# Optimization experiments

Hardware: AMD Instinct MI355X
Metric: run time of the kernel (lower is better)

Reference implementation:

```python
import jax, jax.numpy as jnp
import numpy as np

EMBED_DIM = 1024
N_HEADS = 16
HEAD_DIM = EMBED_DIM // N_HEADS
BATCH = 2
SEQ = 2048


def setup_inputs() -> dict:
    key = jax.random.key(0)
    ks = jax.random.split(key, 12)
    s = 1.0 / np.sqrt(EMBED_DIM)
    return {
        "x": jax.random.normal(ks[0], (BATCH, SEQ, EMBED_DIM), jnp.float32),
        "q_w": jax.random.normal(ks[1], (EMBED_DIM, EMBED_DIM), jnp.float32) * s,
        "q_b": jax.random.normal(ks[2], (EMBED_DIM,), jnp.float32) * s,
        "k_w": jax.random.normal(ks[3], (EMBED_DIM, EMBED_DIM), jnp.float32) * s,
        "k_b": jax.random.normal(ks[4], (EMBED_DIM,), jnp.float32) * s,
        "v_w": jax.random.normal(ks[5], (EMBED_DIM, EMBED_DIM), jnp.float32) * s,
        "v_b": jax.random.normal(ks[6], (EMBED_DIM,), jnp.float32) * s,
        "phase": jax.random.normal(ks[7], (N_HEADS, HEAD_DIM), jnp.float32),
        "entanglement": jax.random.normal(ks[8], (N_HEADS, HEAD_DIM, HEAD_DIM), jnp.float32) * 0.1,
        "out_w": jax.random.normal(ks[9], (EMBED_DIM, EMBED_DIM), jnp.float32) * s,
        "out_b": jax.random.normal(ks[10], (EMBED_DIM,), jnp.float32) * s,
    }


def reference(x, q_w, q_b, k_w, k_b, v_w, v_b, phase, entanglement, out_w, out_b):
    b, s, _ = x.shape
    # projections -> [b, h, s, d]
    def split_heads(y):
        return y.reshape(b, s, N_HEADS, HEAD_DIM).transpose(0, 2, 1, 3)
    Q = split_heads(x @ q_w + q_b)
    K = split_heads(x @ k_w + k_b)
    V = split_heads(x @ v_w + v_b)
    # real part of phase-rotated Q/K: Q * cos(phase) (imag discarded by .real)
    cosp = jnp.cos(phase)[None, :, None, :]  # [1, h, 1, d]
    Qc = Q * cosp
    Kc = K * cosp
    scores = jnp.einsum('bhqd,bhkd->bhqk', Qc, Kc) / np.sqrt(HEAD_DIM)
    # bilinear entanglement term: Q . E . K^T per head
    scores = scores + jnp.einsum('bhqd,hde,bhke->bhqk', Q, entanglement, K)
    attn = jax.nn.softmax(scores, axis=-1)
    attended = jnp.einsum('bhqk,bhkd->bhqd', attn, V)
    attended = attended.transpose(0, 2, 1, 3).reshape(b, s, EMBED_DIM)
    return attended @ out_w + out_b
```

## Files before the change

### kernel.cpp

```cpp
#include <hip/hip_runtime.h>
#include <hip/hip_bf16.h>

typedef __bf16 bf16;
typedef __bf16 bf16x8 __attribute__((ext_vector_type(8)));
typedef __bf16 bf16x4 __attribute__((ext_vector_type(4)));
typedef float f32x4 __attribute__((ext_vector_type(4)));
typedef float f32x16 __attribute__((ext_vector_type(16)));
typedef unsigned int u32x2 __attribute__((ext_vector_type(2)));

#define EMBED 1024
#define NH 16
#define HD 64
#define BATCH 2
#define SEQ 2048
#define MTOK 4096
#define LOG2E 1.4426950408889634f

static __device__ __forceinline__ float fast_exp2(float x) {
#if __has_builtin(__builtin_amdgcn_exp2f)
  return __builtin_amdgcn_exp2f(x);
#else
  float r;
  asm("v_exp_f32 %0, %1" : "=v"(r) : "v"(x));
  return r;
#endif
}

static __device__ __forceinline__ f32x4 mfma16(bf16x8 a, bf16x8 b, f32x4 c) {
  return __builtin_amdgcn_mfma_f32_16x16x32_bf16(a, b, c, 0, 0, 0);
}
static __device__ __forceinline__ f32x16 mfma32(bf16x8 a, bf16x8 b, f32x16 c) {
  return __builtin_amdgcn_mfma_f32_32x32x16_bf16(a, b, c, 0, 0, 0);
}

static __device__ __forceinline__ void gld_lds16(const bf16* g, bf16* l) {
  __builtin_amdgcn_global_load_lds(
      (const __attribute__((address_space(1))) void*)g,
      (__attribute__((address_space(3))) void*)l, 16, 0, 0);
}

__global__ __launch_bounds__(256) void prep_kernel(
    const float* __restrict__ x, const float* __restrict__ qw,
    const float* __restrict__ qb, const float* __restrict__ kw,
    const float* __restrict__ vw, const float* __restrict__ ow,
    const float* __restrict__ ent, const float* __restrict__ phase,
    bf16* __restrict__ xb, bf16* __restrict__ wtall, bf16* __restrict__ wot,
    float* __restrict__ beff) {
  __shared__ float t0[64][65];
  __shared__ float t1[64][65];
  const int bb = blockIdx.x;
  const int tid = threadIdx.x;

  if (bb < 2048) {
    const int n4 = MTOK * EMBED / 4;
    int i = bb * 256 + tid;
    for (; i < n4; i += 2048 * 256) {
      f32x4 v = ((const f32x4*)x)[i];
      bf16x4 o;
      o[0] = (bf16)v[0]; o[1] = (bf16)v[1]; o[2] = (bf16)v[2]; o[3] = (bf16)v[3];
      ((bf16x4*)xb)[i] = o;
    }
    return;
  }
  if (bb < 2816) {
    const int idx = (bb - 2048) & 255;
    const float* W = (bb < 2304) ? kw : (bb < 2560) ? vw : ow;
    bf16* Wt = (bb < 2304) ? (wtall + 1024 * 1024)
             : (bb < 2560) ? (wtall + 2 * 1024 * 1024) : wot;
    const int bc = (idx & 15) * 64;
    const int br = (idx >> 4) * 64;
#pragma unroll
    for (int j = 0; j < 16; j++) {
      int id2 = j * 256 + tid;
      int r = id2 >> 6, c = id2 & 63;
      t0[r][c] = W[(size_t)(br + r) * EMBED + bc + c];
    }
    __syncthreads();
#pragma unroll
    for (int j = 0; j < 16; j++) {
      int id2 = j * 256 + tid;
      int r = id2 >> 6, c = id2 & 63;
      Wt[(size_t)(bc + r) * EMBED + br + c] = (bf16)t0[c][r];
    }
    return;
  }
  if (bb < 3072) {
    const int idx = bb - 2816;
    const int h = idx >> 4;
    const int ibase = (idx & 15) * 64;
#pragma unroll
    for (int j = 0; j < 16; j++) {
      int id2 = j * 256 + tid;
      int i = id2 >> 6, d = id2 & 63;
      t0[i][d] = qw[(size_t)(ibase + i) * EMBED + h * HD + d];
    }
#pragma unroll
    for (int j = 0; j < 16; j++) {
      int id2 = j * 256 + tid;
      int d = id2 >> 6, e = id2 & 63;
      float v = ent[((size_t)h * HD + d) * HD + e];
      if (d == e) { float cp = cosf(phase[h * HD + d]); v += cp * cp * 0.125f; }
      t1[d][e] = v * LOG2E;
    }
    __syncthreads();
    const int i = tid & 63;
    const int e0 = (tid >> 6) * 16;
    float s[16];
#pragma unroll
    for (int ee = 0; ee < 16; ee++) s[ee] = 0.f;
    for (int d = 0; d < 64; d++) {
      float qv = t0[i][d];
#pragma unroll
      for (int ee = 0; ee < 16; ee++) s[ee] += qv * t1[d][e0 + ee];
    }
#pragma unroll
    for (int ee = 0; ee < 16; ee++)
      wtall[(size_t)(h * HD + e0 + ee) * EMBED + ibase + i] = (bf16)s[ee];
    return;
  }
  const int h = bb - 3072;
  if (tid < 64) {
    const int e = tid;
    float s = 0.f;
    for (int d = 0; d < 64; d++) {
      float v = ent[((size_t)h * HD + d) * HD + e];
      if (d == e) { float cp = cosf(phase[h * HD + d]); v += cp * cp * 0.125f; }
      s += qb[h * HD + d] * v;
    }
    beff[h * HD + e] = s * LOG2E;
  }
}

__global__ __launch_bounds__(256, 4) void gemm_qkv_kernel(
    const bf16* __restrict__ A, const bf16* __restrict__ Bt,
    const float* __restrict__ bias_q, const float* __restrict__ bias_k,
    const float* __restrict__ bias_v,
    bf16* __restrict__ Qp, bf16* __restrict__ Kp, bf16* __restrict__ Vt) {
  const int tid = threadIdx.x;
  const int lane = tid & 63, w = tid >> 6;
  const int g = lane >> 4, r15 = lane & 15;
  const int wr = w >> 1, wc = w & 1;

  const int flat = blockIdx.x;
  const int bm = (flat & 31) * 128;
  const int bn = (flat >> 5) * 128;
  const int seg = bn >> 10;

  __shared__ bf16 sA[128 * 32];
  __shared__ bf16 sB[128 * 32];

  const int srow = tid >> 2;
  const int scol = (tid & 3) << 3;
  const bf16* aptr = A + (size_t)(bm + srow) * EMBED + scol;
  const bf16* bptr = Bt + (size_t)(bn + srow) * EMBED + scol;
  bf16* la = sA + tid * 8;
  bf16* lb = sB + tid * 8;

  if (seg == 2) {
    f32x4 acc[4][4];
#pragma unroll
    for (int m = 0; m < 4; m++)
#pragma unroll
      for (int n = 0; n < 4; n++) acc[m][n] = (f32x4){0.f, 0.f, 0.f, 0.f};

    for (int k0 = 0; k0 < EMBED; k0 += 32) {
      __syncthreads();
      gld_lds16(aptr + k0, la);
      gld_lds16(aptr + k0 + 64 * EMBED, la + 64 * 32);
      gld_lds16(bptr + k0, lb);
      gld_lds16(bptr + k0 + 64 * EMBED, lb + 64 * 32);
      __syncthreads();
      bf16x8 af[4], bfv[4];
#pragma unroll
      for (int m = 0; m < 4; m++)
        af[m] = *(const bf16x8*)&sA[(wr * 64 + m * 16 + r15) * 32 + g * 8];
#pragma unroll
      for (int n = 0; n < 4; n++)
        bfv[n] = *(const bf16x8*)&sB[(wc * 64 + n * 16 + r15) * 32 + g * 8];
#pragma unroll
      for (int m = 0; m < 4; m++)
#pragma unroll
        for (int n = 0; n < 4; n++) acc[m][n] = mfma16(af[m], bfv[n], acc[m][n]);
    }

    const int clb = (bn & 1023) + wc * 64;
    const int orow0 = bm + wr * 64;
#pragma unroll
    for (int n = 0; n < 4; n++) {
      const int cl = clb + n * 16 + r15;
      const float bias = bias_v[cl];
      const int hh = cl >> 6, d = cl & 63;
#pragma unroll
      for (int m = 0; m < 4; m++) {
        const int row0 = orow0 + m * 16 + g * 4;
        const int b = row0 >> 11, s = row0 & 2047;
        bf16x4 pk;
#pragma unroll
        for (int r = 0; r < 4; r++) pk[r] = (bf16)(acc[m][n][r] + bias);
        *(bf16x4*)(Vt + ((size_t)((b * NH + hh) * HD + d)) * SEQ + s) = pk;
      }
    }
  } else {
    f32x4 acc[4][4];
#pragma unroll
    for (int m = 0; m < 4; m++)
#pragma unroll
      for (int n = 0; n < 4; n++) acc[m][n] = (f32x4){0.f, 0.f, 0.f, 0.f};

    for (int k0 = 0; k0 < EMBED; k0 += 32) {
      __syncthreads();
      gld_lds16(aptr + k0, la);
      gld_lds16(aptr + k0 + 64 * EMBED, la + 64 * 32);
      gld_lds16(bptr + k0, lb);
      gld_lds16(bptr + k0 + 64 * EMBED, lb + 64 * 32);
      __syncthreads();
      bf16x8 af[4], bfv[4];
#pragma unroll
      for (int m = 0; m < 4; m++)
        af[m] = *(const bf16x8*)&sA[(wr * 64 + m * 16 + r15) * 32 + g * 8];
#pragma unroll
      for (int n = 0; n < 4; n++)
        bfv[n] = *(const bf16x8*)&sB[(wc * 64 + n * 16 + r15) * 32 + g * 8];
#pragma unroll
      for (int m = 0; m < 4; m++)
#pragma unroll
        for (int n = 0; n < 4; n++) acc[m][n] = mfma16(bfv[n], af[m], acc[m][n]);
    }

    const float* bias = seg ? bias_k : bias_q;
    bf16* dst = seg ? Kp : Qp;
    const int clb = (bn & 1023) + wc * 64;
#pragma unroll
    for (int n = 0; n < 4; n++) {
      const int cl4 = clb + n * 16 + g * 4;
      const f32x4 b4 = *(const f32x4*)&bias[cl4];
#pragma unroll
      for (int m = 0; m < 4; m++) {
        const int tr = bm + wr * 64 + m * 16 + r15;
        bf16x4 pk;
#pragma unroll
        for (int r = 0; r < 4; r++) pk[r] = (bf16)(acc[m][n][r] + b4[r]);
        *(bf16x4*)(dst + (size_t)tr * EMBED + cl4) = pk;
      }
    }
  }
}

__global__ __launch_bounds__(256, 4) void gemm_out_kernel(
    const bf16* __restrict__ A, const bf16* __restrict__ Bt,
    const float* __restrict__ bias_o, float* __restrict__ FO) {
  const int tid = threadIdx.x;
  const int lane = tid & 63, w = tid >> 6;
  const int g = lane >> 4, r15 = lane & 15;

  const int flat = blockIdx.x;
  const int bm = (flat & 63) * 64;
  const int bn = (flat >> 6) * 128;

  __shared__ bf16 sA[64 * 32];
  __shared__ bf16 sB[128 * 32];

  f32x4 acc[4][2];
#pragma unroll
  for (int m = 0; m < 4; m++)
#pragma unroll
    for (int n = 0; n < 2; n++) acc[m][n] = (f32x4){0.f, 0.f, 0.f, 0.f};

  const int srow = tid >> 2;
  const int scol = (tid & 3) << 3;
  const bf16* aptr = A + (size_t)(bm + srow) * EMBED + scol;
  const bf16* bptr = Bt + (size_t)(bn + srow) * EMBED + scol;
  bf16* la = sA + tid * 8;
  bf16* lb = sB + tid * 8;

  for (int k0 = 0; k0 < EMBED; k0 += 32) {
    __syncthreads();
    gld_lds16(aptr + k0, la);
    gld_lds16(bptr + k0, lb);
    gld_lds16(bptr + k0 + 64 * EMBED, lb + 64 * 32);
    __syncthreads();
    bf16x8 af[4], bfv[2];
#pragma unroll
    for (int m = 0; m < 4; m++)
      af[m] = *(const bf16x8*)&sA[(m * 16 + r15) * 32 + g * 8];
#pragma unroll
    for (int n = 0; n < 2; n++)
      bfv[n] = *(const bf16x8*)&sB[(w * 32 + n * 16 + r15) * 32 + g * 8];
#pragma unroll
    for (int m = 0; m < 4; m++)
#pragma unroll
      for (int n = 0; n < 2; n++) acc[m][n] = mfma16(bfv[n], af[m], acc[m][n]);
  }

#pragma unroll
  for (int n = 0; n < 2; n++) {
    const int cl4 = bn + w * 32 + n * 16 + g * 4;
    const f32x4 b4 = *(const f32x4*)&bias_o[cl4];
#pragma unroll
    for (int m = 0; m < 4; m++) {
      const int tr = bm + m * 16 + r15;
      *(f32x4*)(FO + (size_t)tr * EMBED + cl4) = acc[m][n] + b4;
    }
  }
}

__global__ __launch_bounds__(512, 4) void flash_attn_kernel(
    const bf16* __restrict__ Qp, const bf16* __restrict__ Kp,
    const bf16* __restrict__ Vt, bf16* __restrict__ Op) {
  const int tid = threadIdx.x, lane = tid & 63, w = tid >> 6;
  const int q31 = lane & 31, hi = lane >> 5;
  const int half = w >> 2, wq = w & 3;
  const int flat = blockIdx.x;
  const int c = (flat & 7) * 64 + (flat >> 3);
  const int bh = c >> 4, qt = c & 15;
  const int b = bh >> 4, h = bh & 15;

  __shared__ char smem[65536];
  bf16* sKb = (bf16*)smem;
  bf16* sVb = (bf16*)(smem + 32768);

  const int g256 = tid & 255;
  const int strow = g256 >> 3;
  const int stcb = (g256 & 7) << 4;

  const char* kgbase = (const char*)(Kp + ((size_t)b * SEQ) * EMBED + h * HD);
  const char* vgbase = (const char*)(Vt + (size_t)bh * HD * SEQ);

  auto stage = [&](int buf, int kv0) {
    bf16* kd = sKb + (size_t)(half * 2 + buf) * 4096 + g256 * 8;
    bf16* vd = sVb + (size_t)(half * 2 + buf) * 4096 + g256 * 8;
#pragma unroll
    for (int i = 0; i < 2; i++) {
      const int row = i * 32 + strow;
      const int sb = stcb ^ ((row & 7) << 4);
      gld_lds16((const bf16*)(kgbase + (size_t)(kv0 + row) * (EMBED * 2) + sb),
                kd + i * 2048);
      gld_lds16((const bf16*)(vgbase + (size_t)row * (SEQ * 2) + (size_t)kv0 * 2 + sb),
                vd + i * 2048);
    }
  };

  const int kvbase = half * 1024;
  stage(0, kvbase);

  const int qbase = qt * 128 + wq * 32;
  const int qrow = qbase + q31;
  const bf16* qptr = Qp + ((size_t)(b * SEQ + qrow)) * EMBED + h * HD;
  bf16x8 aq[4];
#pragma unroll
  for (int ds = 0; ds < 4; ds++)
    aq[ds] = *(const bf16x8*)(qptr + ds * 16 + hi * 8);

  const int sz = (q31 & 7) << 4;
  int cofs[4];
#pragma unroll
  for (int i = 0; i < 4; i++) cofs[i] = ((i * 32 + hi * 16) ^ sz);

  f32x16 o0, o1;
#pragma unroll
  for (int i = 0; i < 16; i++) { o0[i] = 0.f; o1[i] = 0.f; }
  float mrow = -3.0e38f, lrow = 0.f;

  union B4 { bf16x4 v; unsigned int u[2]; };

  for (int it = 0; it < 16; ++it) {
    const int cur = it & 1;
    if (it + 1 < 16) {
      stage(cur ^ 1, kvbase + (it + 1) * 64);
      asm volatile("s_waitcnt vmcnt(4)" ::: "memory");
    } else {
      asm volatile("s_waitcnt vmcnt(0)" ::: "memory");
    }
    __builtin_amdgcn_s_barrier();

    const char* kc = (const char*)(sKb + (size_t)(half * 2 + cur) * 4096) + q31 * 128;
    const char* vc = (const char*)(sVb + (size_t)(half * 2 + cur) * 4096) + q31 * 128;

    f32x16 s0, s1;
#pragma unroll
    for (int i = 0; i < 16; i++) { s0[i] = 0.f; s1[i] = 0.f; }
    __builtin_amdgcn_s_setprio(1);
#pragma unroll
    for (int ds = 0; ds < 4; ds++) {
      bf16x8 bk0 = *(const bf16x8*)(kc + cofs[ds]);
      bf16x8 bk1 = *(const bf16x8*)(kc + 4096 + cofs[ds]);
      s0 = mfma32(bk0, aq[ds], s0);
      s1 = mfma32(bk1, aq[ds], s1);
    }
    __builtin_amdgcn_s_setprio(0);

    float mt = s0[0];
#pragma unroll
    for (int i = 1; i < 16; i++) mt = fmaxf(mt, s0[i]);
#pragma unroll
    for (int i = 0; i < 16; i++) mt = fmaxf(mt, s1[i]);
    {
      u32x2 sm = __builtin_amdgcn_permlane32_swap(__float_as_uint(mt),
                                                  __float_as_uint(mt), false, false);
      mt = fmaxf(__uint_as_float(sm.x), __uint_as_float(sm.y));
    }
    if (__any(mt > mrow + 8.f)) {
      const float mn = fmaxf(mrow, mt);
      const float al = fast_exp2(mrow - mn);
      mrow = mn;
      lrow *= al;
      o0 *= al;
      o1 *= al;
    }

    B4 qd[8];
    float lsum = 0.f;
#pragma unroll
    for (int j = 0; j < 4; j++)
#pragma unroll
      for (int r = 0; r < 4; r++) {
        float pv = fast_exp2(s0[4 * j + r] - mrow);
        lsum += pv;
        qd[j].v[r] = (bf16)pv;
      }
#pragma unroll
    for (int j = 0; j < 4; j++)
#pragma unroll
      for (int r = 0; r < 4; r++) {
        float pv = fast_exp2(s1[4 * j + r] - mrow);
        lsum += pv;
        qd[4 + j].v[r] = (bf16)pv;
      }
    {
      u32x2 ss = __builtin_amdgcn_permlane32_swap(__float_as_uint(lsum),
                                                  __float_as_uint(lsum), false, false);
      lrow += __uint_as_float(ss.x) + __uint_as_float(ss.y);
    }

    bf16x8 pfrag[4];
#pragma unroll
    for (int kt = 0; kt < 4; kt++) {
      u32x2 p0 = __builtin_amdgcn_permlane32_swap(qd[2 * kt].u[0],
                                                  qd[2 * kt + 1].u[0], false, false);
      u32x2 p1 = __builtin_amdgcn_permlane32_swap(qd[2 * kt].u[1],
                                                  qd[2 * kt + 1].u[1], false, false);
      union { unsigned int u[4]; bf16x8 v; } f;
      f.u[0] = p0.x; f.u[1] = p1.x; f.u[2] = p0.y; f.u[3] = p1.y;
      pfrag[kt] = f.v;
    }

    __builtin_amdgcn_s_setprio(1);
#pragma unroll
    for (int kt = 0; kt < 4; kt++) {
      bf16x8 av0 = *(const bf16x8*)(vc + cofs[kt]);
      bf16x8 av1 = *(const bf16x8*)(vc + 4096 + cofs[kt]);
      o0 = mfma32(av0, pfrag[kt], o0);
      o1 = mfma32(av1, pfrag[kt], o1);
    }
    __builtin_amdgcn_s_setprio(0);
    __builtin_amdgcn_s_barrier();
  }

  float* shO = (float*)smem;
  float* shML = (float*)(smem + 33792);
  if (half == 1) {
    float* o = shO + (size_t)(wq * 64 + lane) * 33;
#pragma unroll
    for (int i = 0; i < 16; i++) { o[i] = o0[i]; o[16 + i] = o1[i]; }
    shML[(wq * 64 + lane) * 2] = mrow;
    shML[(wq * 64 + lane) * 2 + 1] = lrow;
  }
  __syncthreads();
  if (half == 0) {
    const float* o = shO + (size_t)(wq * 64 + lane) * 33;
    const float mB = shML[(wq * 64 + lane) * 2];
    const float lB = shML[(wq * 64 + lane) * 2 + 1];
    const float M = fmaxf(mrow, mB);
    const float wA = fast_exp2(mrow - M), wB = fast_exp2(mB - M);
    const float inv = 1.f / (lrow * wA + lB * wB);
    const float fA = wA * inv, fB = wB * inv;

    bf16* obase = Op + ((size_t)(b * SEQ + qrow)) * EMBED + h * HD;
#pragma unroll
    for (int j = 0; j < 4; j++) {
      bf16x4 st;
#pragma unroll
      for (int r = 0; r < 4; r++)
        st[r] = (bf16)(o0[4 * j + r] * fA + o[4 * j + r] * fB);
      *(bf16x4*)(obase + 8 * j + 4 * hi) = st;
    }
#pragma unroll
    for (int j = 0; j < 4; j++) {
      bf16x4 st;
#pragma unroll
      for (int r = 0; r < 4; r++)
        st[r] = (bf16)(o1[4 * j + r] * fA + o[16 + 4 * j + r] * fB);
      *(bf16x4*)(obase + 32 + 8 * j + 4 * hi) = st;
    }
  }
}

extern "C" void kernel_launch(void* const* d_in, const int* in_sizes, int n_in,
                              void* d_out, int out_size, void* d_ws, size_t ws_size,
                              hipStream_t stream) {
  const float* x     = (const float*)d_in[0];
  const float* q_w   = (const float*)d_in[1];
  const float* q_b   = (const float*)d_in[2];
  const float* k_w   = (const float*)d_in[3];
  const float* k_b   = (const float*)d_in[4];
  const float* v_w   = (const float*)d_in[5];
  const float* v_b   = (const float*)d_in[6];
  const float* phase = (const float*)d_in[7];
  const float* ent   = (const float*)d_in[8];
  const float* out_w = (const float*)d_in[9];
  const float* out_b = (const float*)d_in[10];
  float* out = (float*)d_out;

  char* ws = (char*)d_ws;
  bf16* xb    = (bf16*)(ws + 0);
  bf16* wtall = (bf16*)(ws + 8388608);
  bf16* wot   = (bf16*)(ws + 14680064);
  float* beff = (float*)(ws + 16777216);
  bf16* Qp    = (bf16*)(ws + 16781312);
  bf16* Kp    = (bf16*)(ws + 25169920);
  bf16* Vt    = (bf16*)(ws + 33558528);
  (void)in_sizes; (void)n_in; (void)out_size; (void)ws_size;

  prep_kernel<<<3088, 256, 0, stream>>>(x, q_w, q_b, k_w, v_w, out_w, ent, phase,
                                        xb, wtall, wot, beff);

  gemm_qkv_kernel<<<768, 256, 0, stream>>>(
      xb, wtall, beff, k_b, v_b, Qp, Kp, Vt);

  flash_attn_kernel<<<512, 512, 0, stream>>>(Qp, Kp, Vt, xb);

  gemm_out_kernel<<<512, 256, 0, stream>>>(xb, wot, out_b, out);
}
```

Before: 136.1 us.

## Software-pipeline QK^T of next tile with softmax and PV of current tile

Restructures the attention inner loop so the QK^T MFMAs for tile it+1 are issued before the softmax and PV work of tile it, using two ping-ponged score register sets and a loop unrolled by two. K and V staging are split so each buffer is refilled as soon as its last reader is done. Exponentiation, permlane packing and PV MFMAs are interleaved per k-subtile, and the row max becomes a tree reduction to shorten dependency chains. In exchange it uses more registers, which could lower occupancy. It also waits on vmcnt(0) every iteration, which may expose global-load latency the previous vmcnt(4) scheme partly hid.

Result: slower. 154.7 us (+13.6%).

```diff
diff --git a/kernel.cpp b/kernel.cpp
--- a/kernel.cpp
+++ b/kernel.cpp
@@ -326,22 +326,28 @@
   const char* kgbase = (const char*)(Kp + ((size_t)b * SEQ) * EMBED + h * HD);
   const char* vgbase = (const char*)(Vt + (size_t)bh * HD * SEQ);
 
-  auto stage = [&](int buf, int kv0) {
+  auto stageK = [&](int buf, int kv0) {
     bf16* kd = sKb + (size_t)(half * 2 + buf) * 4096 + g256 * 8;
-    bf16* vd = sVb + (size_t)(half * 2 + buf) * 4096 + g256 * 8;
 #pragma unroll
     for (int i = 0; i < 2; i++) {
       const int row = i * 32 + strow;
       const int sb = stcb ^ ((row & 7) << 4);
       gld_lds16((const bf16*)(kgbase + (size_t)(kv0 + row) * (EMBED * 2) + sb),
                 kd + i * 2048);
+    }
+  };
+  auto stageV = [&](int buf, int kv0) {
+    bf16* vd = sVb + (size_t)(half * 2 + buf) * 4096 + g256 * 8;
+#pragma unroll
+    for (int i = 0; i < 2; i++) {
+      const int row = i * 32 + strow;
+      const int sb = stcb ^ ((row & 7) << 4);
       gld_lds16((const bf16*)(vgbase + (size_t)row * (SEQ * 2) + (size_t)kv0 * 2 + sb),
                 vd + i * 2048);
     }
   };
 
   const int kvbase = half * 1024;
-  stage(0, kvbase);
 
   const int qbase = qt * 128 + wq * 32;
   const int qrow = qbase + q31;
@@ -363,37 +369,40 @@
 
   union B4 { bf16x4 v; unsigned int u[2]; };
 
-  for (int it = 0; it < 16; ++it) {
-    const int cur = it & 1;
-    if (it + 1 < 16) {
-      stage(cur ^ 1, kvbase + (it + 1) * 64);
-      asm volatile("s_waitcnt vmcnt(4)" ::: "memory");
-    } else {
-      asm volatile("s_waitcnt vmcnt(0)" ::: "memory");
-    }
-    __builtin_amdgcn_s_barrier();
-
-    const char* kc = (const char*)(sKb + (size_t)(half * 2 + cur) * 4096) + q31 * 128;
-    const char* vc = (const char*)(sVb + (size_t)(half * 2 + cur) * 4096) + q31 * 128;
-
-    f32x16 s0, s1;
-#pragma unroll
-    for (int i = 0; i < 16; i++) { s0[i] = 0.f; s1[i] = 0.f; }
+  auto qk = [&](int it, f32x16& x0, f32x16& x1) {
+    const char* kc = (const char*)(sKb + (size_t)(half * 2 + (it & 1)) * 4096)
+                     + q31 * 128;
+    f32x16 z0, z1;
+#pragma unroll
+    for (int i = 0; i < 16; i++) { z0[i] = 0.f; z1[i] = 0.f; }
     __builtin_amdgcn_s_setprio(1);
 #pragma unroll
     for (int ds = 0; ds < 4; ds++) {
       bf16x8 bk0 = *(const bf16x8*)(kc + cofs[ds]);
       bf16x8 bk1 = *(const bf16x8*)(kc + 4096 + cofs[ds]);
-      s0 = mfma32(bk0, aq[ds], s0);
-      s1 = mfma32(bk1, aq[ds], s1);
+      z0 = mfma32(bk0, aq[ds], z0);
+      z1 = mfma32(bk1, aq[ds], z1);
     }
     __builtin_amdgcn_s_setprio(0);
-
-    float mt = s0[0];
-#pragma unroll
-    for (int i = 1; i < 16; i++) mt = fmaxf(mt, s0[i]);
-#pragma unroll
-    for (int i = 0; i < 16; i++) mt = fmaxf(mt, s1[i]);
+    x0 = z0;
+    x1 = z1;
+  };
+
+  auto smpv = [&](int it, f32x16& c0, f32x16& c1) {
+    float t[11];
+#pragma unroll
+    for (int i = 0; i < 5; i++)
+      t[i] = fmaxf(fmaxf(c0[3 * i], c0[3 * i + 1]), c0[3 * i + 2]);
+    t[5] = fmaxf(fmaxf(c0[15], c1[0]), c1[1]);
+#pragma unroll
+    for (int i = 0; i < 4; i++)
+      t[6 + i] = fmaxf(fmaxf(c1[2 + 3 * i], c1[3 + 3 * i]), c1[4 + 3 * i]);
+    t[10] = fmaxf(c1[14], c1[15]);
+    const float u0 = fmaxf(fmaxf(t[0], t[1]), t[2]);
+    const float u1 = fmaxf(fmaxf(t[3], t[4]), t[5]);
+    const float u2 = fmaxf(fmaxf(t[6], t[7]), t[8]);
+    const float u3 = fmaxf(fmaxf(t[9], t[10]), u0);
+    float mt = fmaxf(fmaxf(u1, u2), u3);
     {
       u32x2 sm = __builtin_amdgcn_permlane32_swap(__float_as_uint(mt),
                                                   __float_as_uint(mt), false, false);
@@ -408,52 +417,71 @@
       o1 *= al;
     }
 
-    B4 qd[8];
+    const char* vc = (const char*)(sVb + (size_t)(half * 2 + (it & 1)) * 4096)
+                     + q31 * 128;
     float lsum = 0.f;
-#pragma unroll
-    for (int j = 0; j < 4; j++)
+    __builtin_amdgcn_s_setprio(1);
+#pragma unroll
+    for (int kt = 0; kt < 4; kt++) {
+      const f32x16& xs = (kt < 2) ? c0 : c1;
+      const int jb = (kt & 1) * 2;
+      B4 q0, q1;
 #pragma unroll
       for (int r = 0; r < 4; r++) {
-        float pv = fast_exp2(s0[4 * j + r] - mrow);
-        lsum += pv;
-        qd[j].v[r] = (bf16)pv;
+        float pa = fast_exp2(xs[4 * jb + r] - mrow);
+        float pb = fast_exp2(xs[4 * (jb + 1) + r] - mrow);
+        lsum += pa + pb;
+        q0.v[r] = (bf16)pa;
+        q1.v[r] = (bf16)pb;
       }
-#pragma unroll
-    for (int j = 0; j < 4; j++)
-#pragma unroll
-      for (int r = 0; r < 4; r++) {
-        float pv = fast_exp2(s1[4 * j + r] - mrow);
-        lsum += pv;
-        qd[4 + j].v[r] = (bf16)pv;
-      }
+      u32x2 p0 = __builtin_amdgcn_permlane32_swap(q0.u[0], q1.u[0], false, false);
+      u32x2 p1 = __builtin_amdgcn_permlane32_swap(q0.u[1], q1.u[1], false, false);
+      union { unsigned int u[4]; bf16x8 v; } f;
+      f.u[0] = p0.x; f.u[1] = p1.x; f.u[2] = p0.y; f.u[3] = p1.y;
+      bf16x8 av0 = *(const bf16x8*)(vc + cofs[kt]);
+      bf16x8 av1 = *(const bf16x8*)(vc + 4096 + cofs[kt]);
+      o0 = mfma32(av0, f.v, o0);
+      o1 = mfma32(av1, f.v, o1);
+    }
+    __builtin_amdgcn_s_setprio(0);
     {
       u32x2 ss = __builtin_amdgcn_permlane32_swap(__float_as_uint(lsum),
                                                   __float_as_uint(lsum), false, false);
       lrow += __uint_as_float(ss.x) + __uint_as_float(ss.y);
     }
-
-    bf16x8 pfrag[4];
-#pragma unroll
-    for (int kt = 0; kt < 4; kt++) {
-      u32x2 p0 = __builtin_amdgcn_permlane32_swap(qd[2 * kt].u[0],
-                                                  qd[2 * kt + 1].u[0], false, false);
-      u32x2 p1 = __builtin_amdgcn_permlane32_swap(qd[2 * kt].u[1],
-                                                  qd[2 * kt + 1].u[1], false, false);
-      union { unsigned int u[4]; bf16x8 v; } f;
-      f.u[0] = p0.x; f.u[1] = p1.x; f.u[2] = p0.y; f.u[3] = p1.y;
-      pfrag[kt] = f.v;
-    }
-
-    __builtin_amdgcn_s_setprio(1);
-#pragma unroll
-    for (int kt = 0; kt < 4; kt++) {
-      bf16x8 av0 = *(const bf16x8*)(vc + cofs[kt]);
-      bf16x8 av1 = *(const bf16x8*)(vc + 4096 + cofs[kt]);
-      o0 = mfma32(av0, pfrag[kt], o0);
-      o1 = mfma32(av1, pfrag[kt], o1);
-    }
-    __builtin_amdgcn_s_setprio(0);
-    __builtin_amdgcn_s_barrier();
+  };
+
+  stageK(0, kvbase);
+  stageV(0, kvbase);
+  stageK(1, kvbase + 64);
+  stageV(1, kvbase + 64);
+  asm volatile("s_waitcnt vmcnt(0)" ::: "memory");
+  __builtin_amdgcn_s_barrier();
+
+  f32x16 sa0, sa1, sb0, sb1;
+  qk(0, sa0, sa1);
+  __builtin_amdgcn_s_barrier();
+
+#pragma unroll
+  for (int ii = 0; ii < 8; ii++) {
+    {
+      const int it = 2 * ii;
+      if (it < 15) qk(it + 1, sb0, sb1);
+      if (it < 14) stageK(it & 1, kvbase + (it + 2) * 64);
+      smpv(it, sa0, sa1);
+      asm volatile("s_waitcnt vmcnt(0)" ::: "memory");
+      __builtin_amdgcn_s_barrier();
+      if (it < 14) stageV(it & 1, kvbase + (it + 2) * 64);
+    }
+    {
+      const int it = 2 * ii + 1;
+      if (it < 15) qk(it + 1, sa0, sa1);
+      if (it < 14) stageK(it & 1, kvbase + (it + 2) * 64);
+      smpv(it, sb0, sb1);
+      asm volatile("s_waitcnt vmcnt(0)" ::: "memory");
+      __builtin_amdgcn_s_barrier();
+      if (it < 14) stageV(it & 1, kvbase + (it + 2) * 64);
+    }
   }
 
   float* shO = (float*)smem;
```

## Software-pipeline flash attention by splitting KV tiles into halves

Applied to the files above, without the earlier changes.

Restructures the flash-attention inner loop so each 64-key tile is processed as two 32-key halves. The QK MFMA of the next half overlaps with the softmax and PV of the current half, and the QK of the next tile is issued before the current tile's second softmax. Staging moves to a two-tile lookahead issued after the barrier, with a full vmcnt(0) wait each iteration. The intent is to hide exp/permlane latency behind MFMA work. The cost is more online-softmax rescale checks, extra barriers, and register pressure from the fully unrolled loop.

After: 138.1 us. About the same (+1.4%).

```diff
diff --git a/kernel.cpp b/kernel.cpp
--- a/kernel.cpp
+++ b/kernel.cpp
@@ -304,6 +304,71 @@
   }
 }
 
+
+#define QK_HALF(CUR, SEL, Z)                                                   \
+  do {                                                                         \
+    const char* kc_ = (const char*)(sKb + (size_t)(half * 2 + (CUR)) * 4096) + \
+                      q31 * 128 + (SEL) * 4096;                                \
+    __builtin_amdgcn_s_setprio(1);                                             \
+    _Pragma("unroll") for (int ds_ = 0; ds_ < 4; ds_++) {                      \
+      bf16x8 bk_ = *(const bf16x8*)(kc_ + cofs[ds_]);                          \
+      Z = mfma32(bk_, aq[ds_], Z);                                             \
+    }                                                                          \
+    __builtin_amdgcn_s_setprio(0);                                             \
+  } while (0)
+
+#define SMPV_HALF(CUR, SEL, S)                                                 \
+  do {                                                                         \
+    float t0_ = fmaxf(fmaxf(S[0], S[1]), S[2]);                                \
+    float t1_ = fmaxf(fmaxf(S[3], S[4]), S[5]);                                \
+    float t2_ = fmaxf(fmaxf(S[6], S[7]), S[8]);                                \
+    float t3_ = fmaxf(fmaxf(S[9], S[10]), S[11]);                              \
+    float t4_ = fmaxf(fmaxf(S[12], S[13]), S[14]);                             \
+    float u0_ = fmaxf(fmaxf(t0_, t1_), t2_);                                   \
+    float u1_ = fmaxf(fmaxf(t3_, t4_), S[15]);                                 \
+    float mt_ = fmaxf(u0_, u1_);                                               \
+    u32x2 sm_ = __builtin_amdgcn_permlane32_swap(                              \
+        __float_as_uint(mt_), __float_as_uint(mt_), false, false);             \
+    mt_ = fmaxf(__uint_as_float(sm_.x), __uint_as_float(sm_.y));               \
+    if (__any(mt_ > mrow + 8.f)) {                                             \
+      const float mn_ = fmaxf(mrow, mt_);                                      \
+      const float al_ = fast_exp2(mrow - mn_);                                 \
+      mrow = mn_;                                                              \
+      lrow *= al_;                                                             \
+      o0 *= al_;                                                               \
+      o1 *= al_;                                                               \
+    }                                                                          \
+    const char* vc_ = (const char*)(sVb + (size_t)(half * 2 + (CUR)) * 4096) + \
+                      q31 * 128;                                               \
+    float lsum_ = 0.f;                                                         \
+    _Pragma("unroll") for (int kk_ = 0; kk_ < 2; kk_++) {                      \
+      const int jb_ = kk_ * 2;                                                 \
+      B4 q0_, q1_;                                                             \
+      _Pragma("unroll") for (int r_ = 0; r_ < 4; r_++) {                       \
+        float pa_ = fast_exp2(S[4 * jb_ + r_] - mrow);                         \
+        float pb_ = fast_exp2(S[4 * jb_ + 4 + r_] - mrow);                     \
+        lsum_ += pa_ + pb_;                                                    \
+        q0_.v[r_] = (bf16)pa_;                                                 \
+        q1_.v[r_] = (bf16)pb_;                                                 \
+      }                                                                        \
+      u32x2 p0_ = __builtin_amdgcn_permlane32_swap(q0_.u[0], q1_.u[0],         \
+                                                   false, false);              \
+      u32x2 p1_ = __builtin_amdgcn_permlane32_swap(q0_.u[1], q1_.u[1],         \
+                                                   false, false);              \
+      union { unsigned int u[4]; bf16x8 v; } f_;                               \
+      f_.u[0] = p0_.x; f_.u[1] = p1_.x; f_.u[2] = p0_.y; f_.u[3] = p1_.y;      \
+      bf16x8 av0_ = *(const bf16x8*)(vc_ + cofs[2 * (SEL) + kk_]);             \
+      bf16x8 av1_ = *(const bf16x8*)(vc_ + 4096 + cofs[2 * (SEL) + kk_]);      \
+      __builtin_amdgcn_s_setprio(1);                                           \
+      o0 = mfma32(av0_, f_.v, o0);                                             \
+      o1 = mfma32(av1_, f_.v, o1);                                             \
+      __builtin_amdgcn_s_setprio(0);                                           \
+    }                                                                          \
+    u32x2 ss_ = __builtin_amdgcn_permlane32_swap(                              \
+        __float_as_uint(lsum_), __float_as_uint(lsum_), false, false);         \
+    lrow += __uint_as_float(ss_.x) + __uint_as_float(ss_.y);                   \
+  } while (0)
+
 __global__ __launch_bounds__(512, 4) void flash_attn_kernel(
     const bf16* __restrict__ Qp, const bf16* __restrict__ Kp,
     const bf16* __restrict__ Vt, bf16* __restrict__ Op) {
@@ -326,22 +391,28 @@
   const char* kgbase = (const char*)(Kp + ((size_t)b * SEQ) * EMBED + h * HD);
   const char* vgbase = (const char*)(Vt + (size_t)bh * HD * SEQ);
 
-  auto stage = [&](int buf, int kv0) {
+  auto stageK = [&](int buf, int kv0) {
     bf16* kd = sKb + (size_t)(half * 2 + buf) * 4096 + g256 * 8;
-    bf16* vd = sVb + (size_t)(half * 2 + buf) * 4096 + g256 * 8;
 #pragma unroll
     for (int i = 0; i < 2; i++) {
       const int row = i * 32 + strow;
       const int sb = stcb ^ ((row & 7) << 4);
       gld_lds16((const bf16*)(kgbase + (size_t)(kv0 + row) * (EMBED * 2) + sb),
                 kd + i * 2048);
+    }
+  };
+  auto stageV = [&](int buf, int kv0) {
+    bf16* vd = sVb + (size_t)(half * 2 + buf) * 4096 + g256 * 8;
+#pragma unroll
+    for (int i = 0; i < 2; i++) {
+      const int row = i * 32 + strow;
+      const int sb = stcb ^ ((row & 7) << 4);
       gld_lds16((const bf16*)(vgbase + (size_t)row * (SEQ * 2) + (size_t)kv0 * 2 + sb),
                 vd + i * 2048);
     }
   };
 
   const int kvbase = half * 1024;
-  stage(0, kvbase);
 
   const int qbase = qt * 128 + wq * 32;
   const int qrow = qbase + q31;
@@ -363,97 +434,38 @@
 
   union B4 { bf16x4 v; unsigned int u[2]; };
 
+  stageK(0, kvbase);
+  stageV(0, kvbase);
+  stageK(1, kvbase + 64);
+  stageV(1, kvbase + 64);
+  asm volatile("s_waitcnt vmcnt(0)" ::: "memory");
+  __builtin_amdgcn_s_barrier();
+
+  f32x16 sA, sB;
+#pragma unroll
+  for (int i = 0; i < 16; i++) sA[i] = 0.f;
+  QK_HALF(0, 0, sA);
+
+#pragma unroll
   for (int it = 0; it < 16; ++it) {
     const int cur = it & 1;
-    if (it + 1 < 16) {
-      stage(cur ^ 1, kvbase + (it + 1) * 64);
-      asm volatile("s_waitcnt vmcnt(4)" ::: "memory");
-    } else {
-      asm volatile("s_waitcnt vmcnt(0)" ::: "memory");
-    }
+#pragma unroll
+    for (int i = 0; i < 16; i++) sB[i] = 0.f;
+    QK_HALF(cur, 1, sB);
+    SMPV_HALF(cur, 0, sA);
+    asm volatile("s_waitcnt vmcnt(0)" ::: "memory");
     __builtin_amdgcn_s_barrier();
-
-    const char* kc = (const char*)(sKb + (size_t)(half * 2 + cur) * 4096) + q31 * 128;
-    const char* vc = (const char*)(sVb + (size_t)(half * 2 + cur) * 4096) + q31 * 128;
-
-    f32x16 s0, s1;
-#pragma unroll
-    for (int i = 0; i < 16; i++) { s0[i] = 0.f; s1[i] = 0.f; }
-    __builtin_amdgcn_s_setprio(1);
-#pragma unroll
-    for (int ds = 0; ds < 4; ds++) {
-      bf16x8 bk0 = *(const bf16x8*)(kc + cofs[ds]);
-      bf16x8 bk1 = *(const bf16x8*)(kc + 4096 + cofs[ds]);
-      s0 = mfma32(bk0, aq[ds], s0);
-      s1 = mfma32(bk1, aq[ds], s1);
-    }
-    __builtin_amdgcn_s_setprio(0);
-
-    float mt = s0[0];
-#pragma unroll
-    for (int i = 1; i < 16; i++) mt = fmaxf(mt, s0[i]);
-#pragma unroll
-    for (int i = 0; i < 16; i++) mt = fmaxf(mt, s1[i]);
-    {
-      u32x2 sm = __builtin_amdgcn_permlane32_swap(__float_as_uint(mt),
-                                                  __float_as_uint(mt), false, false);
-      mt = fmaxf(__uint_as_float(sm.x), __uint_as_float(sm.y));
-    }
-    if (__any(mt > mrow + 8.f)) {
-      const float mn = fmaxf(mrow, mt);
-      const float al = fast_exp2(mrow - mn);
-      mrow = mn;
-      lrow *= al;
-      o0 *= al;
-      o1 *= al;
-    }
-
-    B4 qd[8];
-    float lsum = 0.f;
-#pragma unroll
-    for (int j = 0; j < 4; j++)
-#pragma unroll
-      for (int r = 0; r < 4; r++) {
-        float pv = fast_exp2(s0[4 * j + r] - mrow);
-        lsum += pv;
-        qd[j].v[r] = (bf16)pv;
-      }
-#pragma unroll
-    for (int j = 0; j < 4; j++)
-#pragma unroll
-      for (int r = 0; r < 4; r++) {
-        float pv = fast_exp2(s1[4 * j + r] - mrow);
-        lsum += pv;
-        qd[4 + j].v[r] = (bf16)pv;
-      }
-    {
-      u32x2 ss = __builtin_amdgcn_permlane32_swap(__float_as_uint(lsum),
-                                                  __float_as_uint(lsum), false, false);
-      lrow += __uint_as_float(ss.x) + __uint_as_float(ss.y);
-    }
-
-    bf16x8 pfrag[4];
-#pragma unroll
-    for (int kt = 0; kt < 4; kt++) {
-      u32x2 p0 = __builtin_amdgcn_permlane32_swap(qd[2 * kt].u[0],
-                                                  qd[2 * kt + 1].u[0], false, false);
-      u32x2 p1 = __builtin_amdgcn_permlane32_swap(qd[2 * kt].u[1],
-                                                  qd[2 * kt + 1].u[1], false, false);
-      union { unsigned int u[4]; bf16x8 v; } f;
-      f.u[0] = p0.x; f.u[1] = p1.x; f.u[2] = p0.y; f.u[3] = p1.y;
-      pfrag[kt] = f.v;
-    }
-
-    __builtin_amdgcn_s_setprio(1);
-#pragma unroll
-    for (int kt = 0; kt < 4; kt++) {
-      bf16x8 av0 = *(const bf16x8*)(vc + cofs[kt]);
-      bf16x8 av1 = *(const bf16x8*)(vc + 4096 + cofs[kt]);
-      o0 = mfma32(av0, pfrag[kt], o0);
-      o1 = mfma32(av1, pfrag[kt], o1);
-    }
-    __builtin_amdgcn_s_setprio(0);
+    if (it < 15) {
+#pragma unroll
+      for (int i = 0; i < 16; i++) sA[i] = 0.f;
+      QK_HALF(cur ^ 1, 0, sA);
+    }
+    SMPV_HALF(cur, 1, sB);
     __builtin_amdgcn_s_barrier();
+    if (it < 14) {
+      stageK(cur, kvbase + (it + 2) * 64);
+      stageV(cur, kvbase + (it + 2) * 64);
+    }
   }
 
   float* shO = (float*)smem;
```

## Triple-buffer LDS staging in QKV GEMM to overlap loads with MFMA

Applied to the files above, without the earlier changes.

Turns the QKV projection GEMM's single LDS buffer into a three-stage ring. The next K-slice is prefetched via direct global-to-LDS loads before computing on the current one. A vmcnt wait plus one barrier per iteration replaces the two __syncthreads, hiding global load latency behind MFMA work. LDS use triples to 48KB per block, which may cut occupancy from the requested 4 blocks per CU.

Result: slower. 142.6 us (+4.8%).

```diff
diff --git a/kernel.cpp b/kernel.cpp
--- a/kernel.cpp
+++ b/kernel.cpp
@@ -146,41 +146,52 @@
   const int bn = (flat >> 5) * 128;
   const int seg = bn >> 10;
 
-  __shared__ bf16 sA[128 * 32];
-  __shared__ bf16 sB[128 * 32];
+  __shared__ bf16 sA[3][128 * 32];
+  __shared__ bf16 sB[3][128 * 32];
 
   const int srow = tid >> 2;
   const int scol = (tid & 3) << 3;
   const bf16* aptr = A + (size_t)(bm + srow) * EMBED + scol;
   const bf16* bptr = Bt + (size_t)(bn + srow) * EMBED + scol;
-  bf16* la = sA + tid * 8;
-  bf16* lb = sB + tid * 8;
+
+  auto stage = [&](int buf, int k0) {
+    gld_lds16(aptr + k0, &sA[buf][tid * 8]);
+    gld_lds16(aptr + k0 + 64 * EMBED, &sA[buf][64 * 32 + tid * 8]);
+    gld_lds16(bptr + k0, &sB[buf][tid * 8]);
+    gld_lds16(bptr + k0 + 64 * EMBED, &sB[buf][64 * 32 + tid * 8]);
+  };
+
+  stage(0, 0);
+
+  f32x4 acc[4][4];
+#pragma unroll
+  for (int m = 0; m < 4; m++)
+#pragma unroll
+    for (int n = 0; n < 4; n++) acc[m][n] = (f32x4){0.f, 0.f, 0.f, 0.f};
 
   if (seg == 2) {
-    f32x4 acc[4][4];
-#pragma unroll
-    for (int m = 0; m < 4; m++)
-#pragma unroll
-      for (int n = 0; n < 4; n++) acc[m][n] = (f32x4){0.f, 0.f, 0.f, 0.f};
-
-    for (int k0 = 0; k0 < EMBED; k0 += 32) {
-      __syncthreads();
-      gld_lds16(aptr + k0, la);
-      gld_lds16(aptr + k0 + 64 * EMBED, la + 64 * 32);
-      gld_lds16(bptr + k0, lb);
-      gld_lds16(bptr + k0 + 64 * EMBED, lb + 64 * 32);
-      __syncthreads();
+    int cb = 0;
+    for (int t = 0; t < 32; ++t) {
+      const int nb = (cb == 2) ? 0 : cb + 1;
+      if (t + 1 < 32) {
+        stage(nb, (t + 1) * 32);
+        asm volatile("s_waitcnt vmcnt(4)" ::: "memory");
+      } else {
+        asm volatile("s_waitcnt vmcnt(0)" ::: "memory");
+      }
+      __builtin_amdgcn_s_barrier();
       bf16x8 af[4], bfv[4];
 #pragma unroll
       for (int m = 0; m < 4; m++)
-        af[m] = *(const bf16x8*)&sA[(wr * 64 + m * 16 + r15) * 32 + g * 8];
+        af[m] = *(const bf16x8*)&sA[cb][(wr * 64 + m * 16 + r15) * 32 + g * 8];
 #pragma unroll
       for (int n = 0; n < 4; n++)
-        bfv[n] = *(const bf16x8*)&sB[(wc * 64 + n * 16 + r15) * 32 + g * 8];
+        bfv[n] = *(const bf16x8*)&sB[cb][(wc * 64 + n * 16 + r15) * 32 + g * 8];
 #pragma unroll
       for (int m = 0; m < 4; m++)
 #pragma unroll
         for (int n = 0; n < 4; n++) acc[m][n] = mfma16(af[m], bfv[n], acc[m][n]);
+      cb = nb;
     }
 
     const int clb = (bn & 1023) + wc * 64;
@@ -201,30 +212,28 @@
       }
     }
   } else {
-    f32x4 acc[4][4];
-#pragma unroll
-    for (int m = 0; m < 4; m++)
-#pragma unroll
-      for (int n = 0; n < 4; n++) acc[m][n] = (f32x4){0.f, 0.f, 0.f, 0.f};
-
-    for (int k0 = 0; k0 < EMBED; k0 += 32) {
-      __syncthreads();
-      gld_lds16(aptr + k0, la);
-      gld_lds16(aptr + k0 + 64 * EMBED, la + 64 * 32);
-      gld_lds16(bptr + k0, lb);
-      gld_lds16(bptr + k0 + 64 * EMBED, lb + 64 * 32);
-      __syncthreads();
+    int cb = 0;
+    for (int t = 0; t < 32; ++t) {
+      const int nb = (cb == 2) ? 0 : cb + 1;
+      if (t + 1 < 32) {
+        stage(nb, (t + 1) * 32);
+        asm volatile("s_waitcnt vmcnt(4)" ::: "memory");
+      } else {
+        asm volatile("s_waitcnt vmcnt(0)" ::: "memory");
+      }
+      __builtin_amdgcn_s_barrier();
       bf16x8 af[4], bfv[4];
 #pragma unroll
       for (int m = 0; m < 4; m++)
-        af[m] = *(const bf16x8*)&sA[(wr * 64 + m * 16 + r15) * 32 + g * 8];
+        af[m] = *(const bf16x8*)&sA[cb][(wr * 64 + m * 16 + r15) * 32 + g * 8];
 #pragma unroll
       for (int n = 0; n < 4; n++)
-        bfv[n] = *(const bf16x8*)&sB[(wc * 64 + n * 16 + r15) * 32 + g * 8];
+        bfv[n] = *(const bf16x8*)&sB[cb][(wc * 64 + n * 16 + r15) * 32 + g * 8];
 #pragma unroll
       for (int m = 0; m < 4; m++)
 #pragma unroll
         for (int n = 0; n < 4; n++) acc[m][n] = mfma16(bfv[n], af[m], acc[m][n]);
+      cb = nb;
     }
 
     const float* bias = seg ? bias_k : bias_q;
```
